# Performance work log

Measured on AMD Instinct MI355X. Metric: run time of the kernel, lower is better.

Reference implementation:

```python
import jax, jax.numpy as jnp
import numpy as np
import math

D = 1024      # input/embed dim
H = 16        # heads
HD = D // H   # head dim
FF = 4096     # feedforward dim
B, S = 2, 2048
LN_EPS = 1e-5
NEG = -9e15


def setup_inputs() -> dict:
    key = jax.random.key(0)
    ks = jax.random.split(key, 16)
    inp = {
        "x": jax.random.normal(ks[0], (B, S, D), jnp.float32),
        "mask": jax.random.randint(ks[1], (1, 1, S, S), 0, 2, jnp.int32),
        "pos_bias": jax.random.normal(ks[2], (1, H, S, S), jnp.float32),
        "sinusoidal_pos": jax.random.normal(ks[3], (1, 1, S, HD), jnp.float32),
        # params (xavier-ish scale)
        "Wqkv": jax.random.normal(ks[4], (D, 3 * D), jnp.float32) * math.sqrt(2.0 / (D + 3 * D)),
        "bqkv": jnp.zeros((3 * D,), jnp.float32),
        "Wo": jax.random.normal(ks[5], (D, D), jnp.float32) * math.sqrt(1.0 / D),
        "bo": jnp.zeros((D,), jnp.float32),
        "W1": jax.random.normal(ks[6], (D, FF), jnp.float32) * math.sqrt(2.0 / (D + FF)),
        "b1": jnp.zeros((FF,), jnp.float32),
        "W2": jax.random.normal(ks[7], (FF, D), jnp.float32) * math.sqrt(2.0 / (D + FF)),
        "b2": jnp.zeros((D,), jnp.float32),
        "g1": jnp.ones((D,), jnp.float32),
        "be1": jnp.zeros((D,), jnp.float32),
        "g2": jnp.ones((D,), jnp.float32),
        "be2": jnp.zeros((D,), jnp.float32),
    }
    return inp


def _layernorm(x, g, b):
    mu = jnp.mean(x, axis=-1, keepdims=True)
    var = jnp.mean(jnp.square(x - mu), axis=-1, keepdims=True)
    return (x - mu) * jax.lax.rsqrt(var + LN_EPS) * g + b


def _rotate_half(x):
    # x: [..., HD] -> reshape [..., 2, HD//2], swap with negation, concat
    r = x.reshape(*x.shape[:-1], 2, -1)
    x1, x2 = r[..., 0, :], r[..., 1, :]
    return jnp.concatenate([-x2, x1], axis=-1)


def _rope(x, sp):
    # sp: [1,1,S,HD]; x: [B,H,S,HD]
    return x * jnp.cos(sp) + _rotate_half(x) * jnp.sin(sp)


def reference(x, mask, pos_bias, sinusoidal_pos, Wqkv, bqkv, Wo, bo,
              W1, b1, W2, b2, g1, be1, g2, be2):
    # pre-norm (note: residual uses the normalized x, matching the source)
    x = _layernorm(x, g1, be1)
    b, s, d = x.shape
    qkv = (x @ Wqkv + bqkv).reshape(b, s, H, 3 * HD).transpose(0, 2, 1, 3)
    q, k, v = jnp.split(qkv, 3, axis=-1)  # each [B,H,S,HD]
    sp = sinusoidal_pos[:, :, -s:]
    q = _rope(q, sp)
    k = _rope(k, sp)
    logits = jnp.einsum("bhqd,bhkd->bhqk", q, k)
    logits = (logits + pos_bias) / math.sqrt(HD)
    logits = jnp.where(mask == 0, NEG, logits)
    attn = jax.nn.softmax(logits, axis=-1)
    vals = jnp.einsum("bhqk,bhkd->bhqd", attn, v)
    vals = vals.transpose(0, 2, 1, 3).reshape(b, s, d)
    attn_out = vals @ Wo + bo
    x = x + attn_out
    x = _layernorm(x, g2, be2)
    h = jax.nn.gelu(x @ W1 + b1, approximate=False)  # torch GELU is exact
    x = x + (h @ W2 + b2)
    return x
```

## Files before the change

### kernel.cpp

```cpp
#include <hip/hip_runtime.h>
#include <math.h>

#define DD   1024
#define HH   16
#define HDD  64
#define FFF  4096
#define NB   2
#define NS   2048
#define NR   (NB * NS)
#define TDQ  (3 * DD)

typedef __attribute__((ext_vector_type(8))) _Float16 hfrag;
typedef __attribute__((ext_vector_type(4))) _Float16 h4v;
typedef __attribute__((ext_vector_type(4))) float f32x4;
typedef __attribute__((ext_vector_type(16))) float f32x16;
typedef __attribute__((ext_vector_type(8))) unsigned short us8;

__device__ __forceinline__ float4 ld4(const float* p) {
    return *reinterpret_cast<const float4*>(p);
}
__device__ __forceinline__ float gelu_f(float x) {
    return 0.5f * x * (1.0f + erff(x * 0.70710678118654752440f));
}
#define MFMA32H(a, b, c) __builtin_amdgcn_mfma_f32_32x32x16_f16((a), (b), (c), 0, 0, 0)

__global__ __launch_bounds__(256) void ln_kernel(const float* __restrict__ in,
        const float* __restrict__ gw, const float* __restrict__ bw,
        float* __restrict__ outf, _Float16* __restrict__ oh) {
    int row = blockIdx.x;
    float4 v = reinterpret_cast<const float4*>(in + (size_t)row * DD)[threadIdx.x];
    float s1 = v.x + v.y + v.z + v.w;
    float s2 = v.x * v.x + v.y * v.y + v.z * v.z + v.w * v.w;
#pragma unroll
    for (int off = 1; off < 64; off <<= 1) {
        s1 += __shfl_xor(s1, off);
        s2 += __shfl_xor(s2, off);
    }
    __shared__ float r1[4], r2[4];
    int wid = threadIdx.x >> 6;
    if ((threadIdx.x & 63) == 0) { r1[wid] = s1; r2[wid] = s2; }
    __syncthreads();
    s1 = r1[0] + r1[1] + r1[2] + r1[3];
    s2 = r2[0] + r2[1] + r2[2] + r2[3];
    float mu   = s1 * (1.0f / DD);
    float var  = s2 * (1.0f / DD) - mu * mu;
    float rstd = rsqrtf(var + 1e-5f);
    float4 g = reinterpret_cast<const float4*>(gw)[threadIdx.x];
    float4 b = reinterpret_cast<const float4*>(bw)[threadIdx.x];
    float o[4];
    o[0] = (v.x - mu) * rstd * g.x + b.x;
    o[1] = (v.y - mu) * rstd * g.y + b.y;
    o[2] = (v.z - mu) * rstd * g.z + b.z;
    o[3] = (v.w - mu) * rstd * g.w + b.w;
    float4 of; of.x = o[0]; of.y = o[1]; of.z = o[2]; of.w = o[3];
    reinterpret_cast<float4*>(outf + (size_t)row * DD)[threadIdx.x] = of;
    h4v hv;
#pragma unroll
    for (int j = 0; j < 4; ++j) hv[j] = (_Float16)o[j];
    *reinterpret_cast<h4v*>(oh + (size_t)row * DD + threadIdx.x * 4) = hv;
}

__global__ __launch_bounds__(256) void wt_convert(const float* __restrict__ W,
        _Float16* __restrict__ Th, int K, int N) {
    __shared__ float s[32][33];
    int tx = threadIdx.x & 31, ty = threadIdx.x >> 5;
    int n0 = blockIdx.x * 32, k0 = blockIdx.y * 32;
#pragma unroll
    for (int i = 0; i < 4; ++i)
        s[ty + i * 8][tx] = W[(size_t)(k0 + ty + i * 8) * N + n0 + tx];
    __syncthreads();
#pragma unroll
    for (int i = 0; i < 4; ++i) {
        int n = n0 + ty + i * 8;
        Th[(size_t)n * K + k0 + tx] = (_Float16)s[tx][ty + i * 8];
    }
}

__global__ __launch_bounds__(256) void cs_table(const float* __restrict__ sp,
        float* __restrict__ ct, float* __restrict__ st) {
    int i = blockIdx.x * 256 + threadIdx.x;
    float v = sp[i];
    ct[i] = cosf(v);
    st[i] = sinf(v);
}

__global__ __launch_bounds__(256) void mask8(const int* __restrict__ mask,
        unsigned char* __restrict__ mb) {
    int i = blockIdx.x * 256 + threadIdx.x;
    int4 v = reinterpret_cast<const int4*>(mask)[i];
    unsigned int o = (unsigned int)(v.x & 1) | ((unsigned int)(v.y & 1) << 8)
                   | ((unsigned int)(v.z & 1) << 16) | ((unsigned int)(v.w & 1) << 24);
    reinterpret_cast<unsigned int*>(mb)[i] = o;
}

__global__ __launch_bounds__(256) void rope_split(const _Float16* __restrict__ qkv,
        const float* __restrict__ ct, const float* __restrict__ st,
        _Float16* __restrict__ Qp, _Float16* __restrict__ Kp, _Float16* __restrict__ Vt) {
    __shared__ _Float16 sv[64][72];
    const int t = threadIdx.x;
    const int tile = blockIdx.x, bh = blockIdx.y;
    const int b = bh >> 4, h = bh & 15;
    const int r = t >> 2, p = t & 3;
    const int srow = tile * 64 + r;
    const _Float16* base = qkv + ((size_t)(b * NS + srow)) * TDQ + h * 192;

#pragma unroll
    for (int qk = 0; qk < 2; ++qk) {
        const _Float16* src = base + qk * 64;
        hfrag va = *reinterpret_cast<const hfrag*>(src + p * 8);
        hfrag vc = *reinterpret_cast<const hfrag*>(src + 32 + p * 8);
        hfrag o1, o2;
#pragma unroll
        for (int j = 0; j < 8; ++j) {
            int d1 = p * 8 + j, d2 = 32 + p * 8 + j;
            float a = (float)va[j], c = (float)vc[j];
            float c1 = ct[(size_t)srow * HDD + d1], s1 = st[(size_t)srow * HDD + d1];
            float c2 = ct[(size_t)srow * HDD + d2], s2 = st[(size_t)srow * HDD + d2];
            o1[j] = (_Float16)(a * c1 - c * s1);
            o2[j] = (_Float16)(c * c2 + a * s2);
        }
        _Float16* dst = qk ? Kp : Qp;
        size_t obase = ((size_t)bh * NS + srow) * HDD;
        *reinterpret_cast<hfrag*>(dst + obase + p * 8)      = o1;
        *reinterpret_cast<hfrag*>(dst + obase + 32 + p * 8) = o2;
    }
    const _Float16* vsrc = base + 128;
    hfrag v0 = *reinterpret_cast<const hfrag*>(vsrc + p * 16);
    hfrag v1 = *reinterpret_cast<const hfrag*>(vsrc + p * 16 + 8);
#pragma unroll
    for (int j = 0; j < 8; ++j) {
        sv[p * 16 + j][r]     = v0[j];
        sv[p * 16 + 8 + j][r] = v1[j];
    }
    __syncthreads();
    {
        int d = t >> 2, kb = (t & 3) * 16;
        size_t obase = ((size_t)bh * HDD + d) * NS + tile * 64 + kb;
        *reinterpret_cast<hfrag*>(Vt + obase)     = *reinterpret_cast<hfrag*>(&sv[d][kb]);
        *reinterpret_cast<hfrag*>(Vt + obase + 8) = *reinterpret_cast<hfrag*>(&sv[d][kb + 8]);
    }
}

__global__ __launch_bounds__(256) void attn_mfma(
        const _Float16* __restrict__ Qp, const _Float16* __restrict__ Kp,
        const _Float16* __restrict__ Vt,
        const float* __restrict__ pos_bias, const unsigned char* __restrict__ maskb,
        _Float16* __restrict__ valf) {
    __shared__ _Float16 kT[64][72];
    __shared__ _Float16 vT[64][72];
    __shared__ _Float16 pT[4][32][72];
    __shared__ _Float16 PBs[4][32][68];
    const int t = threadIdx.x;
    const int w = t >> 6, lane = t & 63, lq = lane & 31, hi = lane >> 5;
    const int h = blockIdx.y >> 1, b = blockIdx.y & 1;
    const int bh = b * HH + h;
    const int q0 = blockIdx.x * 128;
    const int qg = q0 + 32 * w + lq;
    const int sw = ((lq >> 3) & 3) << 3;
    const float C1  = 0.18033688011112042f;
    const float THR = 11.5f;

    hfrag qf[4];
#pragma unroll
    for (int dk = 0; dk < 4; ++dk)
        qf[dk] = *reinterpret_cast<const hfrag*>(
            Qp + ((size_t)bh * NS + qg) * HDD + 16 * dk + 8 * hi);

    f32x16 o0 = (f32x16)0.0f, o1 = (f32x16)0.0f;
    float mrun = -INFINITY, lsum = 0.0f;

    const int sr0 = t >> 2, sc = t & 3;
    const int swr = ((sr0 >> 3) & 3) << 3;
    const int brow = lane >> 4;
    const int bcol = (lane & 15) * 4;
    us8 kr[2], vr[2];
    float4 pbr[8]; unsigned int pmk[8];

#define STAGE_LOAD(KT) {                                                        \
        int kv0_ = (KT) * 64;                                                   \
        size_t kb_ = ((size_t)bh * NS + kv0_ + sr0) * HDD + 16 * sc;            \
        size_t vb_ = ((size_t)bh * HDD + sr0) * NS + kv0_ + 16 * sc;            \
        kr[0] = *reinterpret_cast<const us8*>(Kp + kb_);                        \
        kr[1] = *reinterpret_cast<const us8*>(Kp + kb_ + 8);                    \
        vr[0] = *reinterpret_cast<const us8*>(Vt + vb_);                        \
        vr[1] = *reinterpret_cast<const us8*>(Vt + vb_ + 8);                    \
        _Pragma("unroll")                                                       \
        for (int i = 0; i < 8; ++i) {                                           \
            int rg_ = q0 + 32 * w + brow + 4 * i;                               \
            pbr[i] = ld4(pos_bias + ((size_t)h * NS + rg_) * NS + kv0_ + bcol); \
            pmk[i] = *reinterpret_cast<const unsigned int*>(                    \
                         maskb + (size_t)rg_ * NS + kv0_ + bcol);               \
        }                                                                       \
    }

    STAGE_LOAD(0);
    for (int kt = 0; kt < NS / 64; ++kt) {
        __syncthreads();
        *reinterpret_cast<us8*>(&kT[sr0][(16 * sc) ^ swr])     = kr[0];
        *reinterpret_cast<us8*>(&kT[sr0][(16 * sc + 8) ^ swr]) = kr[1];
        *reinterpret_cast<us8*>(&vT[sr0][(16 * sc) ^ swr])     = vr[0];
        *reinterpret_cast<us8*>(&vT[sr0][(16 * sc + 8) ^ swr]) = vr[1];
#pragma unroll
        for (int i = 0; i < 8; ++i) {
            h4v pv;
#pragma unroll
            for (int j = 0; j < 4; ++j)
                pv[j] = ((pmk[i] >> (8 * j)) & 0xffu)
                      ? (_Float16)(pbr[i][j] * C1) : (_Float16)(-60000.0f);
            *reinterpret_cast<h4v*>(&PBs[w][brow + 4 * i][bcol]) = pv;
        }
        __syncthreads();
        if (kt + 1 < NS / 64) STAGE_LOAD(kt + 1);

        f32x16 s0 = (f32x16)0.0f, s1 = (f32x16)0.0f;
#pragma unroll
        for (int dk = 0; dk < 4; ++dk) {
            hfrag k0 = *reinterpret_cast<const hfrag*>(&kT[lq][(16 * dk + 8 * hi) ^ sw]);
            hfrag k1 = *reinterpret_cast<const hfrag*>(&kT[32 + lq][(16 * dk + 8 * hi) ^ sw]);
            s0 = MFMA32H(k0, qf[dk], s0);
            s1 = MFMA32H(k1, qf[dk], s1);
        }
        float sv[2][16];
#pragma unroll
        for (int m2 = 0; m2 < 2; ++m2)
#pragma unroll
            for (int g = 0; g < 4; ++g) {
                h4v pb4 = *reinterpret_cast<const h4v*>(&PBs[w][lq][32 * m2 + 8 * g + 4 * hi]);
#pragma unroll
                for (int j = 0; j < 4; ++j) {
                    int r = 4 * g + j;
                    float sraw = (m2 == 0) ? s0[r] : s1[r];
                    sv[m2][r] = fmaf(sraw, C1, (float)pb4[j]);
                }
            }
        float mx = sv[0][0];
#pragma unroll
        for (int m2 = 0; m2 < 2; ++m2)
#pragma unroll
            for (int r = 0; r < 16; ++r) mx = fmaxf(mx, sv[m2][r]);
        mx = fmaxf(mx, __shfl_xor(mx, 32));
        if (__any(mx > mrun + THR)) {
            float mnew = fmaxf(mrun, mx);
            float corr = __builtin_amdgcn_exp2f(mrun - mnew);
            lsum *= corr;
            mrun = mnew;
#pragma unroll
            for (int r = 0; r < 16; ++r) {
                int iq = (r & 3) + 8 * (r >> 2) + 4 * hi;
                float cr = __shfl(corr, iq);
                o0[r] *= cr; o1[r] *= cr;
            }
        }
        float ps = 0.0f;
#pragma unroll
        for (int m2 = 0; m2 < 2; ++m2)
#pragma unroll
            for (int g = 0; g < 4; ++g) {
                float p0 = __builtin_amdgcn_exp2f(sv[m2][4 * g + 0] - mrun);
                float p1 = __builtin_amdgcn_exp2f(sv[m2][4 * g + 1] - mrun);
                float p2 = __builtin_amdgcn_exp2f(sv[m2][4 * g + 2] - mrun);
                float p3 = __builtin_amdgcn_exp2f(sv[m2][4 * g + 3] - mrun);
                ps += p0 + p1 + p2 + p3;
                h4v hp;
                hp[0] = (_Float16)p0; hp[1] = (_Float16)p1;
                hp[2] = (_Float16)p2; hp[3] = (_Float16)p3;
                int koff = (32 * m2 + 8 * g + 4 * hi) ^ sw;
                *reinterpret_cast<h4v*>(&pT[w][lq][koff]) = hp;
            }
        ps += __shfl_xor(ps, 32);
        lsum += ps;
#pragma unroll
        for (int kp = 0; kp < 4; ++kp) {
            hfrag ph = *reinterpret_cast<const hfrag*>(&pT[w][lq][(16 * kp + 8 * hi) ^ sw]);
            hfrag v0 = *reinterpret_cast<const hfrag*>(&vT[lq][(16 * kp + 8 * hi) ^ sw]);
            hfrag v1 = *reinterpret_cast<const hfrag*>(&vT[32 + lq][(16 * kp + 8 * hi) ^ sw]);
            o0 = MFMA32H(ph, v0, o0);
            o1 = MFMA32H(ph, v1, o1);
        }
    }
#undef STAGE_LOAD
    float inv = 1.0f / lsum;
#pragma unroll
    for (int r = 0; r < 16; ++r) {
        int iq = (r & 3) + 8 * (r >> 2) + 4 * hi;
        float ivr = __shfl(inv, iq);
        size_t rowb = ((size_t)(b * NS + q0 + 32 * w + iq)) * DD + h * HDD;
        valf[rowb + lq]      = (_Float16)(o0[r] * ivr);
        valf[rowb + 32 + lq] = (_Float16)(o1[r] * ivr);
    }
}

template<int EPI>
__global__ __launch_bounds__(256, 2) void gemm_h(
        const _Float16* __restrict__ A, const _Float16* __restrict__ B,
        const float* __restrict__ bias, const float* __restrict__ resid,
        float* __restrict__ Cf, _Float16* __restrict__ Ch,
        int M, int N, int K) {
    __shared__ _Float16 sA[128][40];
    __shared__ _Float16 sB[128][40];
    const int t = threadIdx.x;
    const int w = t >> 6, lane = t & 63, lq = lane & 31, hi = lane >> 5;
    const int wr = w >> 1, wc = w & 1;
    const int m0 = blockIdx.y * 128, n0 = blockIdx.x * 128;

    f32x16 acc[2][2];
#pragma unroll
    for (int m = 0; m < 2; ++m)
#pragma unroll
        for (int n = 0; n < 2; ++n) acc[m][n] = (f32x16)0.0f;

    const int sr = t >> 1, skc = (t & 1) * 16;
    const _Float16* Ap = A + (size_t)(m0 + sr) * K + skc;
    const _Float16* Bp = B + (size_t)(n0 + sr) * K + skc;

    for (int k0 = 0; k0 < K; k0 += 32) {
        us8 a0 = *reinterpret_cast<const us8*>(Ap + k0);
        us8 a1 = *reinterpret_cast<const us8*>(Ap + k0 + 8);
        us8 b0 = *reinterpret_cast<const us8*>(Bp + k0);
        us8 b1 = *reinterpret_cast<const us8*>(Bp + k0 + 8);
        __syncthreads();
        *reinterpret_cast<us8*>(&sA[sr][skc])     = a0;
        *reinterpret_cast<us8*>(&sA[sr][skc + 8]) = a1;
        *reinterpret_cast<us8*>(&sB[sr][skc])     = b0;
        *reinterpret_cast<us8*>(&sB[sr][skc + 8]) = b1;
        __syncthreads();
        hfrag fa[2][2], fb[2][2];
#pragma unroll
        for (int mb = 0; mb < 2; ++mb)
#pragma unroll
            for (int kc = 0; kc < 2; ++kc)
                fa[mb][kc] = *reinterpret_cast<const hfrag*>(
                    &sA[wr * 64 + mb * 32 + lq][kc * 16 + 8 * hi]);
#pragma unroll
        for (int nb = 0; nb < 2; ++nb)
#pragma unroll
            for (int kc = 0; kc < 2; ++kc)
                fb[nb][kc] = *reinterpret_cast<const hfrag*>(
                    &sB[wc * 64 + nb * 32 + lq][kc * 16 + 8 * hi]);
#pragma unroll
        for (int kc = 0; kc < 2; ++kc)
#pragma unroll
            for (int mb = 0; mb < 2; ++mb)
#pragma unroll
                for (int nb = 0; nb < 2; ++nb)
                    acc[mb][nb] = MFMA32H(fa[mb][kc], fb[nb][kc], acc[mb][nb]);
    }
#pragma unroll
    for (int mb = 0; mb < 2; ++mb)
#pragma unroll
        for (int nb = 0; nb < 2; ++nb) {
            int colg = n0 + wc * 64 + nb * 32 + lq;
            float bv = bias[colg];
#pragma unroll
            for (int r = 0; r < 16; ++r) {
                int rowg = m0 + wr * 64 + mb * 32 + (r & 3) + 8 * (r >> 2) + 4 * hi;
                float v = acc[mb][nb][r] + bv;
                if (EPI == 1) v += resid[(size_t)rowg * N + colg];
                if (EPI == 2) {
                    Ch[(size_t)rowg * N + colg] = (_Float16)gelu_f(v);
                } else if (EPI == 3) {
                    Ch[(size_t)rowg * N + colg] = (_Float16)v;
                } else {
                    Cf[(size_t)rowg * N + colg] = v;
                }
            }
        }
}

extern "C" void kernel_launch(void* const* d_in, const int* in_sizes, int n_in,
                              void* d_out, int out_size, void* d_ws, size_t ws_size,
                              hipStream_t stream) {
    const float* x        = (const float*)d_in[0];
    const int*   mask     = (const int*)d_in[1];
    const float* pos_bias = (const float*)d_in[2];
    const float* sp       = (const float*)d_in[3];
    const float* Wqkv     = (const float*)d_in[4];
    const float* bqkv     = (const float*)d_in[5];
    const float* Wo       = (const float*)d_in[6];
    const float* bo       = (const float*)d_in[7];
    const float* W1       = (const float*)d_in[8];
    const float* b1       = (const float*)d_in[9];
    const float* W2       = (const float*)d_in[10];
    const float* b2       = (const float*)d_in[11];
    const float* g1       = (const float*)d_in[12];
    const float* be1      = (const float*)d_in[13];
    const float* g2       = (const float*)d_in[14];
    const float* be2      = (const float*)d_in[15];
    float* out = (float*)d_out;
    char* wsb = (char*)d_ws;

    float*          xbuf = (float*)(wsb);
    _Float16*       actF = (_Float16*)(wsb + ((size_t)16 << 20));
    _Float16*       wT   = (_Float16*)(wsb + ((size_t)24 << 20));
    float*          ct   = (float*)(wsb + ((size_t)32 << 20));
    float*          stb  = (float*)(wsb + ((size_t)33 << 20));
    unsigned char*  mkb  = (unsigned char*)(wsb + ((size_t)34 << 20));
    _Float16*       qkvh = (_Float16*)(wsb + ((size_t)48 << 20));
    _Float16*       Qp   = (_Float16*)(wsb + ((size_t)72 << 20));
    _Float16*       Kp   = (_Float16*)(wsb + ((size_t)80 << 20));
    _Float16*       Vt   = (_Float16*)(wsb + ((size_t)88 << 20));
    _Float16*       hF   = (_Float16*)(wsb + ((size_t)48 << 20));

    ln_kernel<<<NR, 256, 0, stream>>>(x, g1, be1, xbuf, actF);
    wt_convert<<<dim3(TDQ / 32, DD / 32), 256, 0, stream>>>(Wqkv, wT, DD, TDQ);
    gemm_h<3><<<dim3(TDQ / 128, NR / 128), 256, 0, stream>>>(
        actF, wT, bqkv, nullptr, nullptr, qkvh, NR, TDQ, DD);
    cs_table<<<(NS * HDD) / 256, 256, 0, stream>>>(sp, ct, stb);
    mask8<<<(NS * NS / 4) / 256, 256, 0, stream>>>(mask, mkb);
    rope_split<<<dim3(NS / 64, NB * HH), 256, 0, stream>>>(qkvh, ct, stb, Qp, Kp, Vt);
    attn_mfma<<<dim3(NS / 128, NB * HH), 256, 0, stream>>>(
        Qp, Kp, Vt, pos_bias, mkb, actF);
    wt_convert<<<dim3(DD / 32, DD / 32), 256, 0, stream>>>(Wo, wT, DD, DD);
    gemm_h<1><<<dim3(DD / 128, NR / 128), 256, 0, stream>>>(
        actF, wT, bo, xbuf, xbuf, nullptr, NR, DD, DD);
    ln_kernel<<<NR, 256, 0, stream>>>(xbuf, g2, be2, xbuf, actF);
    wt_convert<<<dim3(FFF / 32, DD / 32), 256, 0, stream>>>(W1, wT, DD, FFF);
    gemm_h<2><<<dim3(FFF / 128, NR / 128), 256, 0, stream>>>(
        actF, wT, b1, nullptr, nullptr, hF, NR, FFF, DD);
    wt_convert<<<dim3(DD / 32, FFF / 32), 256, 0, stream>>>(W2, wT, FFF, DD);
    gemm_h<1><<<dim3(DD / 128, NR / 128), 256, 0, stream>>>(
        hF, wT, b2, xbuf, out, nullptr, NR, DD, FFF);
}
```

Baseline: 454.3 us.

## Split attention over KV halves, keep P in registers, add 64-row GEMM

The attention kernel now splits the KV range into two halves across a third grid dimension. Partial O, max and sum go to workspace and a new combine kernel merges and normalizes them, which doubles the block count for better CU occupancy. The P matrix is packed into MFMA A-fragments with cvt_pkrtz and cross-half shuffles instead of a round trip through shared memory. The GEMM shared tiles get XOR swizzling against bank conflicts, and the N=1024 GEMMs use a new 64-row-tile kernel for more blocks. The cost is extra fp32 partial-output traffic and one more kernel launch.

After: 627.4 us. +38.1%, slower.

```diff
diff --git a/kernel.cpp b/kernel.cpp
--- a/kernel.cpp
+++ b/kernel.cpp
@@ -12,9 +12,10 @@
 
 typedef __attribute__((ext_vector_type(8))) _Float16 hfrag;
 typedef __attribute__((ext_vector_type(4))) _Float16 h4v;
-typedef __attribute__((ext_vector_type(4))) float f32x4;
+typedef __attribute__((ext_vector_type(2))) _Float16 h2v;
 typedef __attribute__((ext_vector_type(16))) float f32x16;
 typedef __attribute__((ext_vector_type(8))) unsigned short us8;
+typedef __attribute__((ext_vector_type(4))) unsigned int u32x4;
 
 __device__ __forceinline__ float4 ld4(const float* p) {
     return *reinterpret_cast<const float4*>(p);
@@ -141,22 +142,23 @@
     }
 }
 
-__global__ __launch_bounds__(256) void attn_mfma(
+__global__ __launch_bounds__(256, 3) void attn_mfma(
         const _Float16* __restrict__ Qp, const _Float16* __restrict__ Kp,
         const _Float16* __restrict__ Vt,
         const float* __restrict__ pos_bias, const unsigned char* __restrict__ maskb,
-        _Float16* __restrict__ valf) {
+        float* __restrict__ Opart, float2* __restrict__ Lpart) {
     __shared__ _Float16 kT[64][72];
     __shared__ _Float16 vT[64][72];
-    __shared__ _Float16 pT[4][32][72];
     __shared__ _Float16 PBs[4][32][68];
     const int t = threadIdx.x;
     const int w = t >> 6, lane = t & 63, lq = lane & 31, hi = lane >> 5;
     const int h = blockIdx.y >> 1, b = blockIdx.y & 1;
     const int bh = b * HH + h;
-    const int q0 = blockIdx.x * 128;
+    const int qt = blockIdx.x, sp = blockIdx.z;
+    const int q0 = qt * 128;
     const int qg = q0 + 32 * w + lq;
     const int sw = ((lq >> 3) & 3) << 3;
+    const int KT0 = sp * 16, KT1 = KT0 + 16;
     const float C1  = 0.18033688011112042f;
     const float THR = 11.5f;
 
@@ -193,8 +195,8 @@
         }                                                                       \
     }
 
-    STAGE_LOAD(0);
-    for (int kt = 0; kt < NS / 64; ++kt) {
+    STAGE_LOAD(KT0);
+    for (int kt = KT0; kt < KT1; ++kt) {
         __syncthreads();
         *reinterpret_cast<us8*>(&kT[sr0][(16 * sc) ^ swr])     = kr[0];
         *reinterpret_cast<us8*>(&kT[sr0][(16 * sc + 8) ^ swr]) = kr[1];
@@ -210,7 +212,7 @@
             *reinterpret_cast<h4v*>(&PBs[w][brow + 4 * i][bcol]) = pv;
         }
         __syncthreads();
-        if (kt + 1 < NS / 64) STAGE_LOAD(kt + 1);
+        if (kt + 1 < KT1) STAGE_LOAD(kt + 1);
 
         f32x16 s0 = (f32x16)0.0f, s1 = (f32x16)0.0f;
 #pragma unroll
@@ -252,41 +254,89 @@
             }
         }
         float ps = 0.0f;
+        hfrag af[4];
 #pragma unroll
         for (int m2 = 0; m2 < 2; ++m2)
 #pragma unroll
-            for (int g = 0; g < 4; ++g) {
-                float p0 = __builtin_amdgcn_exp2f(sv[m2][4 * g + 0] - mrun);
-                float p1 = __builtin_amdgcn_exp2f(sv[m2][4 * g + 1] - mrun);
-                float p2 = __builtin_amdgcn_exp2f(sv[m2][4 * g + 2] - mrun);
-                float p3 = __builtin_amdgcn_exp2f(sv[m2][4 * g + 3] - mrun);
-                ps += p0 + p1 + p2 + p3;
-                h4v hp;
-                hp[0] = (_Float16)p0; hp[1] = (_Float16)p1;
-                hp[2] = (_Float16)p2; hp[3] = (_Float16)p3;
-                int koff = (32 * m2 + 8 * g + 4 * hi) ^ sw;
-                *reinterpret_cast<h4v*>(&pT[w][lq][koff]) = hp;
+            for (int gp = 0; gp < 2; ++gp) {
+                float p0 = __builtin_amdgcn_exp2f(sv[m2][8 * gp + 0] - mrun);
+                float p1 = __builtin_amdgcn_exp2f(sv[m2][8 * gp + 1] - mrun);
+                float p2 = __builtin_amdgcn_exp2f(sv[m2][8 * gp + 2] - mrun);
+                float p3 = __builtin_amdgcn_exp2f(sv[m2][8 * gp + 3] - mrun);
+                float p4 = __builtin_amdgcn_exp2f(sv[m2][8 * gp + 4] - mrun);
+                float p5 = __builtin_amdgcn_exp2f(sv[m2][8 * gp + 5] - mrun);
+                float p6 = __builtin_amdgcn_exp2f(sv[m2][8 * gp + 6] - mrun);
+                float p7 = __builtin_amdgcn_exp2f(sv[m2][8 * gp + 7] - mrun);
+                ps += (p0 + p1) + (p2 + p3) + (p4 + p5) + (p6 + p7);
+                unsigned int XA = __builtin_bit_cast(unsigned int, __builtin_amdgcn_cvt_pkrtz(p0, p1));
+                unsigned int XB = __builtin_bit_cast(unsigned int, __builtin_amdgcn_cvt_pkrtz(p2, p3));
+                unsigned int XC = __builtin_bit_cast(unsigned int, __builtin_amdgcn_cvt_pkrtz(p4, p5));
+                unsigned int XD = __builtin_bit_cast(unsigned int, __builtin_amdgcn_cvt_pkrtz(p6, p7));
+                unsigned int YA = (unsigned int)__shfl_xor((int)XA, 32);
+                unsigned int YB = (unsigned int)__shfl_xor((int)XB, 32);
+                unsigned int YC = (unsigned int)__shfl_xor((int)XC, 32);
+                unsigned int YD = (unsigned int)__shfl_xor((int)XD, 32);
+                u32x4 aw;
+                aw[0] = hi ? YC : XA;
+                aw[1] = hi ? YD : XB;
+                aw[2] = hi ? XC : YA;
+                aw[3] = hi ? XD : YB;
+                af[m2 * 2 + gp] = __builtin_bit_cast(hfrag, aw);
             }
         ps += __shfl_xor(ps, 32);
         lsum += ps;
 #pragma unroll
         for (int kp = 0; kp < 4; ++kp) {
-            hfrag ph = *reinterpret_cast<const hfrag*>(&pT[w][lq][(16 * kp + 8 * hi) ^ sw]);
             hfrag v0 = *reinterpret_cast<const hfrag*>(&vT[lq][(16 * kp + 8 * hi) ^ sw]);
             hfrag v1 = *reinterpret_cast<const hfrag*>(&vT[32 + lq][(16 * kp + 8 * hi) ^ sw]);
-            o0 = MFMA32H(ph, v0, o0);
-            o1 = MFMA32H(ph, v1, o1);
+            o0 = MFMA32H(af[kp], v0, o0);
+            o1 = MFMA32H(af[kp], v1, o1);
         }
     }
 #undef STAGE_LOAD
-    float inv = 1.0f / lsum;
+    size_t obase = (((size_t)(bh * 16 + qt)) * 2 + sp) * (size_t)(128 * 64);
 #pragma unroll
     for (int r = 0; r < 16; ++r) {
         int iq = (r & 3) + 8 * (r >> 2) + 4 * hi;
-        float ivr = __shfl(inv, iq);
-        size_t rowb = ((size_t)(b * NS + q0 + 32 * w + iq)) * DD + h * HDD;
-        valf[rowb + lq]      = (_Float16)(o0[r] * ivr);
-        valf[rowb + 32 + lq] = (_Float16)(o1[r] * ivr);
+        Opart[obase + (size_t)(32 * w + iq) * 64 + lq]      = o0[r];
+        Opart[obase + (size_t)(32 * w + iq) * 64 + 32 + lq] = o1[r];
+    }
+    if (hi == 0) {
+        float2 ml; ml.x = mrun; ml.y = lsum;
+        Lpart[(((size_t)(bh * 16 + qt)) * 2 + sp) * 128 + 32 * w + lq] = ml;
+    }
+}
+
+__global__ __launch_bounds__(256) void attn_combine(const float* __restrict__ Opart,
+        const float2* __restrict__ Lpart, _Float16* __restrict__ valf) {
+    const int qt = blockIdx.x;
+    const int h = blockIdx.y >> 1, b = blockIdx.y & 1;
+    const int bh = b * HH + h;
+    const int t = threadIdx.x;
+    const int qloc = t >> 2, d0 = (t & 3) * 16;
+    size_t base = ((size_t)(bh * 16 + qt)) * 2;
+#pragma unroll
+    for (int half = 0; half < 2; ++half) {
+        int q = qloc + 64 * half;
+        float2 ml0 = Lpart[(base + 0) * 128 + q];
+        float2 ml1 = Lpart[(base + 1) * 128 + q];
+        float m = fmaxf(ml0.x, ml1.x);
+        float a0 = __builtin_amdgcn_exp2f(ml0.x - m);
+        float a1 = __builtin_amdgcn_exp2f(ml1.x - m);
+        float inv = 1.0f / (ml0.y * a0 + ml1.y * a1);
+        const float* O0 = Opart + (base + 0) * 8192 + (size_t)q * 64 + d0;
+        const float* O1 = Opart + (base + 1) * 8192 + (size_t)q * 64 + d0;
+        _Float16* dst = valf + ((size_t)(b * NS + qt * 128 + q)) * DD + h * HDD + d0;
+#pragma unroll
+        for (int j = 0; j < 4; ++j) {
+            float4 x0 = ld4(O0 + 4 * j), x1 = ld4(O1 + 4 * j);
+            h4v o;
+            o[0] = (_Float16)((x0.x * a0 + x1.x * a1) * inv);
+            o[1] = (_Float16)((x0.y * a0 + x1.y * a1) * inv);
+            o[2] = (_Float16)((x0.z * a0 + x1.z * a1) * inv);
+            o[3] = (_Float16)((x0.w * a0 + x1.w * a1) * inv);
+            *reinterpret_cast<h4v*>(dst + 4 * j) = o;
+        }
     }
 }
 
@@ -296,12 +346,13 @@
         const float* __restrict__ bias, const float* __restrict__ resid,
         float* __restrict__ Cf, _Float16* __restrict__ Ch,
         int M, int N, int K) {
-    __shared__ _Float16 sA[128][40];
-    __shared__ _Float16 sB[128][40];
+    __shared__ _Float16 sA[128][72];
+    __shared__ _Float16 sB[128][72];
     const int t = threadIdx.x;
     const int w = t >> 6, lane = t & 63, lq = lane & 31, hi = lane >> 5;
     const int wr = w >> 1, wc = w & 1;
     const int m0 = blockIdx.y * 128, n0 = blockIdx.x * 128;
+    const int sw = ((lq >> 3) & 3) << 3;
 
     f32x16 acc[2][2];
 #pragma unroll
@@ -310,6 +361,7 @@
         for (int n = 0; n < 2; ++n) acc[m][n] = (f32x16)0.0f;
 
     const int sr = t >> 1, skc = (t & 1) * 16;
+    const int swr = ((sr >> 3) & 3) << 3;
     const _Float16* Ap = A + (size_t)(m0 + sr) * K + skc;
     const _Float16* Bp = B + (size_t)(n0 + sr) * K + skc;
 
@@ -319,10 +371,10 @@
         us8 b0 = *reinterpret_cast<const us8*>(Bp + k0);
         us8 b1 = *reinterpret_cast<const us8*>(Bp + k0 + 8);
         __syncthreads();
-        *reinterpret_cast<us8*>(&sA[sr][skc])     = a0;
-        *reinterpret_cast<us8*>(&sA[sr][skc + 8]) = a1;
-        *reinterpret_cast<us8*>(&sB[sr][skc])     = b0;
-        *reinterpret_cast<us8*>(&sB[sr][skc + 8]) = b1;
+        *reinterpret_cast<us8*>(&sA[sr][(skc) ^ swr])     = a0;
+        *reinterpret_cast<us8*>(&sA[sr][(skc + 8) ^ swr]) = a1;
+        *reinterpret_cast<us8*>(&sB[sr][(skc) ^ swr])     = b0;
+        *reinterpret_cast<us8*>(&sB[sr][(skc + 8) ^ swr]) = b1;
         __syncthreads();
         hfrag fa[2][2], fb[2][2];
 #pragma unroll
@@ -330,13 +382,13 @@
 #pragma unroll
             for (int kc = 0; kc < 2; ++kc)
                 fa[mb][kc] = *reinterpret_cast<const hfrag*>(
-                    &sA[wr * 64 + mb * 32 + lq][kc * 16 + 8 * hi]);
+                    &sA[wr * 64 + mb * 32 + lq][(kc * 16 + 8 * hi) ^ sw]);
 #pragma unroll
         for (int nb = 0; nb < 2; ++nb)
 #pragma unroll
             for (int kc = 0; kc < 2; ++kc)
                 fb[nb][kc] = *reinterpret_cast<const hfrag*>(
-                    &sB[wc * 64 + nb * 32 + lq][kc * 16 + 8 * hi]);
+                    &sB[wc * 64 + nb * 32 + lq][(kc * 16 + 8 * hi) ^ sw]);
 #pragma unroll
         for (int kc = 0; kc < 2; ++kc)
 #pragma unroll
@@ -364,6 +416,65 @@
                     Cf[(size_t)rowg * N + colg] = v;
                 }
             }
+        }
+}
+
+__global__ __launch_bounds__(256, 2) void gemm_h2(
+        const _Float16* __restrict__ A, const _Float16* __restrict__ B,
+        const float* __restrict__ bias, const float* __restrict__ resid,
+        float* __restrict__ Cf, int M, int N, int K) {
+    __shared__ _Float16 sA[64][72];
+    __shared__ _Float16 sB[128][72];
+    const int t = threadIdx.x;
+    const int w = t >> 6, lane = t & 63, lq = lane & 31, hi = lane >> 5;
+    const int m0 = blockIdx.y * 64, n0 = blockIdx.x * 128;
+    const int sw = ((lq >> 3) & 3) << 3;
+
+    f32x16 acc[2];
+    acc[0] = (f32x16)0.0f; acc[1] = (f32x16)0.0f;
+
+    const int ar = t >> 2, akc = (t & 3) * 8;
+    const int aswr = ((ar >> 3) & 3) << 3;
+    const int br = t >> 1, bkc = (t & 1) * 16;
+    const int bswr = ((br >> 3) & 3) << 3;
+    const _Float16* Ap = A + (size_t)(m0 + ar) * K + akc;
+    const _Float16* Bp = B + (size_t)(n0 + br) * K + bkc;
+
+    for (int k0 = 0; k0 < K; k0 += 32) {
+        us8 a0 = *reinterpret_cast<const us8*>(Ap + k0);
+        us8 b0 = *reinterpret_cast<const us8*>(Bp + k0);
+        us8 b1 = *reinterpret_cast<const us8*>(Bp + k0 + 8);
+        __syncthreads();
+        *reinterpret_cast<us8*>(&sA[ar][(akc) ^ aswr])    = a0;
+        *reinterpret_cast<us8*>(&sB[br][(bkc) ^ bswr])    = b0;
+        *reinterpret_cast<us8*>(&sB[br][(bkc + 8) ^ bswr]) = b1;
+        __syncthreads();
+        hfrag fa[2][2], fb[2];
+#pragma unroll
+        for (int mb = 0; mb < 2; ++mb)
+#pragma unroll
+            for (int kc = 0; kc < 2; ++kc)
+                fa[mb][kc] = *reinterpret_cast<const hfrag*>(
+                    &sA[mb * 32 + lq][(kc * 16 + 8 * hi) ^ sw]);
+#pragma unroll
+        for (int kc = 0; kc < 2; ++kc)
+            fb[kc] = *reinterpret_cast<const hfrag*>(
+                &sB[32 * w + lq][(kc * 16 + 8 * hi) ^ sw]);
+#pragma unroll
+        for (int kc = 0; kc < 2; ++kc)
+#pragma unroll
+            for (int mb = 0; mb < 2; ++mb)
+                acc[mb] = MFMA32H(fa[mb][kc], fb[kc], acc[mb]);
+    }
+    int colg = n0 + 32 * w + lq;
+    float bv = bias[colg];
+#pragma unroll
+    for (int mb = 0; mb < 2; ++mb)
+#pragma unroll
+        for (int r = 0; r < 16; ++r) {
+            int rowg = m0 + mb * 32 + (r & 3) + 8 * (r >> 2) + 4 * hi;
+            float v = acc[mb][r] + bv + resid[(size_t)rowg * N + colg];
+            Cf[(size_t)rowg * N + colg] = v;
         }
 }
 
@@ -389,17 +500,19 @@
     float* out = (float*)d_out;
     char* wsb = (char*)d_ws;
 
-    float*          xbuf = (float*)(wsb);
-    _Float16*       actF = (_Float16*)(wsb + ((size_t)16 << 20));
-    _Float16*       wT   = (_Float16*)(wsb + ((size_t)24 << 20));
-    float*          ct   = (float*)(wsb + ((size_t)32 << 20));
-    float*          stb  = (float*)(wsb + ((size_t)33 << 20));
-    unsigned char*  mkb  = (unsigned char*)(wsb + ((size_t)34 << 20));
-    _Float16*       qkvh = (_Float16*)(wsb + ((size_t)48 << 20));
-    _Float16*       Qp   = (_Float16*)(wsb + ((size_t)72 << 20));
-    _Float16*       Kp   = (_Float16*)(wsb + ((size_t)80 << 20));
-    _Float16*       Vt   = (_Float16*)(wsb + ((size_t)88 << 20));
-    _Float16*       hF   = (_Float16*)(wsb + ((size_t)48 << 20));
+    float*          xbuf  = (float*)(wsb);
+    _Float16*       actF  = (_Float16*)(wsb + ((size_t)16 << 20));
+    _Float16*       wT    = (_Float16*)(wsb + ((size_t)24 << 20));
+    float*          ct    = (float*)(wsb + ((size_t)32 << 20));
+    float*          stb   = (float*)(wsb + ((size_t)33 << 20));
+    unsigned char*  mkb   = (unsigned char*)(wsb + ((size_t)34 << 20));
+    _Float16*       qkvh  = (_Float16*)(wsb + ((size_t)48 << 20));
+    _Float16*       Qp    = (_Float16*)(wsb + ((size_t)72 << 20));
+    _Float16*       Kp    = (_Float16*)(wsb + ((size_t)80 << 20));
+    _Float16*       Vt    = (_Float16*)(wsb + ((size_t)88 << 20));
+    _Float16*       hF    = (_Float16*)(wsb + ((size_t)48 << 20));
+    float*          Opart = (float*)(wsb + ((size_t)96 << 20));
+    float2*         Lpart = (float2*)(wsb + ((size_t)130 << 20));
 
     ln_kernel<<<NR, 256, 0, stream>>>(x, g1, be1, xbuf, actF);
     wt_convert<<<dim3(TDQ / 32, DD / 32), 256, 0, stream>>>(Wqkv, wT, DD, TDQ);
@@ -408,16 +521,17 @@
     cs_table<<<(NS * HDD) / 256, 256, 0, stream>>>(sp, ct, stb);
     mask8<<<(NS * NS / 4) / 256, 256, 0, stream>>>(mask, mkb);
     rope_split<<<dim3(NS / 64, NB * HH), 256, 0, stream>>>(qkvh, ct, stb, Qp, Kp, Vt);
-    attn_mfma<<<dim3(NS / 128, NB * HH), 256, 0, stream>>>(
-        Qp, Kp, Vt, pos_bias, mkb, actF);
+    attn_mfma<<<dim3(NS / 128, NB * HH, 2), 256, 0, stream>>>(
+        Qp, Kp, Vt, pos_bias, mkb, Opart, Lpart);
+    attn_combine<<<dim3(NS / 128, NB * HH), 256, 0, stream>>>(Opart, Lpart, actF);
     wt_convert<<<dim3(DD / 32, DD / 32), 256, 0, stream>>>(Wo, wT, DD, DD);
-    gemm_h<1><<<dim3(DD / 128, NR / 128), 256, 0, stream>>>(
-        actF, wT, bo, xbuf, xbuf, nullptr, NR, DD, DD);
+    gemm_h2<<<dim3(DD / 128, NR / 64), 256, 0, stream>>>(
+        actF, wT, bo, xbuf, xbuf, NR, DD, DD);
     ln_kernel<<<NR, 256, 0, stream>>>(xbuf, g2, be2, xbuf, actF);
     wt_convert<<<dim3(FFF / 32, DD / 32), 256, 0, stream>>>(W1, wT, DD, FFF);
     gemm_h<2><<<dim3(FFF / 128, NR / 128), 256, 0, stream>>>(
         actF, wT, b1, nullptr, nullptr, hF, NR, FFF, DD);
     wt_convert<<<dim3(DD / 32, FFF / 32), 256, 0, stream>>>(W2, wT, FFF, DD);
-    gemm_h<1><<<dim3(DD / 128, NR / 128), 256, 0, stream>>>(
-        hF, wT, b2, xbuf, out, nullptr, NR, DD, FFF);
-}
+    gemm_h2<<<dim3(DD / 128, NR / 64), 256, 0, stream>>>(
+        hF, wT, b2, xbuf, out, NR, DD, FFF);
+}
```
